# Kernel tuning notes

Measured on AMD Instinct MI355X. Metric: run time of the kernel, lower is better.

The kernel has to match this reference:

```python
import jax, jax.numpy as jnp
import numpy as np

D_MODEL, N_HEAD, D_HEAD = 1024, 16, 64
QLEN, MLEN, BSZ = 1024, 512, 4
KLEN = QLEN + MLEN
RLEN = QLEN + KLEN
SCALE = 1.0 / (D_HEAD ** 0.5)
LN_EPS = 1e-12


def rel_shift(x, klen):
    # x: [i, j, b, n] -> shifted [i, klen, b, n]
    i, j, b, n = x.shape
    x = x.reshape(j, i, b, n)[1:].reshape(i, j - 1, b, n)
    return x[:, :klen]


def layer_norm(x, gamma, beta, eps=LN_EPS):
    mu = jnp.mean(x, axis=-1, keepdims=True)
    var = jnp.mean(jnp.square(x - mu), axis=-1, keepdims=True)
    return (x - mu) * jax.lax.rsqrt(var + eps) * gamma + beta


def setup_inputs() -> dict:
    key = jax.random.key(0)
    ks = jax.random.split(key, 16)
    std = 0.02
    h = jax.random.normal(ks[0], (QLEN, BSZ, D_MODEL), jnp.float32)
    r = jax.random.normal(ks[1], (RLEN, BSZ, D_MODEL), jnp.float32)
    mems = jax.random.normal(ks[2], (MLEN, BSZ, D_MODEL), jnp.float32)
    # binary float mask (1 = masked), broadcast over head dim
    attn_mask = (jax.random.uniform(ks[3], (QLEN, KLEN, BSZ, 1)) < 0.1).astype(jnp.float32)
    # one-hot segment matrix over 2 segment classes
    seg_ids = jax.random.randint(ks[4], (QLEN, KLEN, BSZ), 0, 2)
    seg_mat = jax.nn.one_hot(seg_ids, 2, dtype=jnp.float32)
    Wq = std * jax.random.normal(ks[5], (D_MODEL, N_HEAD, D_HEAD), jnp.float32)
    Wk = std * jax.random.normal(ks[6], (D_MODEL, N_HEAD, D_HEAD), jnp.float32)
    Wv = std * jax.random.normal(ks[7], (D_MODEL, N_HEAD, D_HEAD), jnp.float32)
    Wo = std * jax.random.normal(ks[8], (D_MODEL, N_HEAD, D_HEAD), jnp.float32)
    Wr = std * jax.random.normal(ks[9], (D_MODEL, N_HEAD, D_HEAD), jnp.float32)
    r_w_bias = jnp.zeros((N_HEAD, D_HEAD), jnp.float32)
    r_r_bias = jnp.zeros((N_HEAD, D_HEAD), jnp.float32)
    r_s_bias = jnp.zeros((N_HEAD, D_HEAD), jnp.float32)
    seg_embed = std * jax.random.normal(ks[10], (2, N_HEAD, D_HEAD), jnp.float32)
    ln_gamma = jnp.ones((D_MODEL,), jnp.float32)
    ln_beta = jnp.zeros((D_MODEL,), jnp.float32)
    return dict(h=h, r=r, mems=mems, attn_mask=attn_mask, seg_mat=seg_mat,
                Wq=Wq, Wk=Wk, Wv=Wv, Wo=Wo, Wr=Wr,
                r_w_bias=r_w_bias, r_r_bias=r_r_bias, r_s_bias=r_s_bias,
                seg_embed=seg_embed, ln_gamma=ln_gamma, ln_beta=ln_beta)


def reference(h, r, mems, attn_mask, seg_mat, Wq, Wk, Wv, Wo, Wr,
              r_w_bias, r_r_bias, r_s_bias, seg_embed, ln_gamma, ln_beta):
    cat = jnp.concatenate([mems, h], axis=0)  # [klen, b, d_model]
    q_head = jnp.einsum('ibh,hnd->ibnd', h, Wq)
    k_head_h = jnp.einsum('jbh,hnd->jbnd', cat, Wk)
    v_head_h = jnp.einsum('jbh,hnd->jbnd', cat, Wv)
    k_head_r = jnp.einsum('jbh,hnd->jbnd', r, Wr)

    klen = k_head_h.shape[0]
    ac = jnp.einsum('ibnd,jbnd->ijbn', q_head + r_w_bias, k_head_h)
    bd = jnp.einsum('ibnd,jbnd->ijbn', q_head + r_r_bias, k_head_r)
    bd = rel_shift(bd, klen)
    ef = jnp.einsum('ibnd,snd->ibns', q_head + r_s_bias, seg_embed)
    ef = jnp.einsum('ijbs,ibns->ijbn', seg_mat, ef)

    attn_score = (ac + bd + ef) * SCALE - 1e30 * attn_mask
    attn_prob = jax.nn.softmax(attn_score, axis=1)
    attn_vec = jnp.einsum('ijbn,jbnd->ibnd', attn_prob, v_head_h)

    attn_out = jnp.einsum('ibnd,hnd->ibh', attn_vec, Wo) + h  # residual
    return layer_norm(attn_out, ln_gamma, ln_beta)
```

## Files before the change

### kernel.cpp

```cpp
#include <hip/hip_runtime.h>

typedef unsigned short u16;
typedef __attribute__((ext_vector_type(8))) short bf16x8;
typedef __attribute__((ext_vector_type(4))) float f32x4;

constexpr int DM = 1024;
constexpr int NH = 16;
constexpr int DH = 64;
constexpr int QL = 1024;
constexpr int ML = 512;
constexpr int KL = 1536;
constexpr int RL = 2560;
constexpr int BS = 4;
constexpr int JT = KL / 64;
constexpr float SCALE = 0.125f;

static __device__ __forceinline__ u16 f2bf(float f) {
    unsigned u = __float_as_uint(f);
    u += 0x7fffu + ((u >> 16) & 1u);
    return (u16)(u >> 16);
}

static __device__ __forceinline__ void glds16(const u16* g, u16* l) {
    __builtin_amdgcn_global_load_lds(
        (const __attribute__((address_space(1))) unsigned int*)g,
        (__attribute__((address_space(3))) unsigned int*)l,
        16, 0, 0);
}

__global__ __launch_bounds__(256) void prep_kernel(
    const float* __restrict__ mems, const float* __restrict__ h,
    const float* __restrict__ r, const float* __restrict__ Wo,
    const float* __restrict__ mask, const float* __restrict__ segm,
    const float* __restrict__ Wq, const float* __restrict__ Wk,
    const float* __restrict__ Wv, const float* __restrict__ Wr,
    u16* __restrict__ catb, u16* __restrict__ rb, u16* __restrict__ wob,
    u16* __restrict__ WqT, u16* __restrict__ WkT,
    u16* __restrict__ WvT, u16* __restrict__ WrT,
    ulonglong2* __restrict__ pk)
{
    __shared__ float smem[64 * 65];
    const int id = blockIdx.x;
    const int t = threadIdx.x;

    if (id < 17408) {
        const long C0 = (long)ML * BS * DM;
        const long C1 = (long)KL * BS * DM;
        const long C2 = C1 + (long)RL * BS * DM;
        long g = ((long)id * 256 + t) * 4;
        const float* src; u16* dst;
        if (g < C0)      { src = mems + g;        dst = catb + g; }
        else if (g < C1) { src = h + (g - C0);    dst = catb + g; }
        else if (g < C2) { src = r + (g - C1);    dst = rb + (g - C1); }
        else             { src = Wo + (g - C2);   dst = wob + (g - C2); }
        float4 v = *(const float4*)src;
        unsigned lo = (unsigned)f2bf(v.x) | ((unsigned)f2bf(v.y) << 16);
        unsigned hi = (unsigned)f2bf(v.z) | ((unsigned)f2bf(v.w) << 16);
        *(uint2*)dst = make_uint2(lo, hi);
        return;
    }
    if (id < 18432) {
        float (*tile)[65] = (float(*)[65])smem;
        const int local = id - 17408;
        const float* W; u16* WT;
        switch (local >> 8) {
            case 0:  W = Wq; WT = WqT; break;
            case 1:  W = Wk; WT = WkT; break;
            case 2:  W = Wv; WT = WvT; break;
            default: W = Wr; WT = WrT; break;
        }
        const int k0 = (local & 15) * 64, n0 = ((local >> 4) & 15) * 64;
        const int tr = t >> 6, tc = t & 63;
        #pragma unroll
        for (int rr = 0; rr < 16; rr++) {
            int rw = tr + rr * 4;
            tile[rw][tc] = W[(size_t)(k0 + rw) * DM + n0 + tc];
        }
        __syncthreads();
        #pragma unroll
        for (int rr = 0; rr < 16; rr++) {
            int n = tr + rr * 4;
            WT[(size_t)(n0 + n) * DM + k0 + tc] = f2bf(tile[tc][n]);
        }
        return;
    }
    {
        float* mk = smem;
        float* sg = smem + 256;
        const int local = id - 18432;
        const int i = local / JT, jt = local - i * JT;
        const size_t base = ((size_t)i * KL + jt * 64) * BS;
        mk[t] = mask[base + t];
        float2 s2 = ((const float2*)(segm + base * 2))[t];
        sg[t] = s2.y;
        __syncthreads();
        const int b = t >> 6, lane = t & 63;
        const unsigned long long mb = __ballot(mk[lane * 4 + b] > 0.5f);
        const unsigned long long sb = __ballot(sg[lane * 4 + b] > 0.5f);
        if (lane == 0) {
            ulonglong2 v; v.x = mb; v.y = sb;
            pk[((size_t)b * QL + i) * JT + jt] = v;
        }
    }
}

__global__ __launch_bounds__(256) void proj_kernel(
    const u16* __restrict__ hb, const u16* __restrict__ catb,
    const u16* __restrict__ rb,
    const u16* __restrict__ WqT, const u16* __restrict__ WkT,
    const u16* __restrict__ WvT, const u16* __restrict__ WrT,
    float* __restrict__ q_s, u16* __restrict__ k_s,
    u16* __restrict__ v_s, u16* __restrict__ kr_s)
{
    __shared__ u16 a_lds[128][32];
    __shared__ u16 b_lds[128][32];
    const int id = blockIdx.x;
    const u16 *A, *B; void* C; int SEQ, MODE, local;
    if (id < 256)       { A = hb;   B = WqT; C = q_s;  SEQ = QL; MODE = 1; local = id; }
    else if (id < 640)  { A = catb; B = WkT; C = k_s;  SEQ = KL; MODE = 2; local = id - 256; }
    else if (id < 1024) { A = catb; B = WvT; C = v_s;  SEQ = KL; MODE = 2; local = id - 640; }
    else                { A = rb;   B = WrT; C = kr_s; SEQ = RL; MODE = 2; local = id - 1024; }
    const int bm = local >> 3, bnn = local & 7;

    const int t = threadIdx.x;
    const int w = t >> 6, lane = t & 63, l15 = lane & 15, q4 = lane >> 4;
    const int wm = (w >> 1) * 64, wn = (w & 1) * 64;
    const int srow = w * 32 + (lane >> 2);
    const int scol = (lane & 3) * 8;
    const u16* Ab = A + (size_t)(bm * 128 + srow) * DM + scol;
    const u16* Bb = B + (size_t)(bnn * 128 + srow) * DM + scol;
    u16* a_dst = &a_lds[w * 32][0];
    u16* b_dst = &b_lds[w * 32][0];

    f32x4 acc[4][4] = {};

    for (int k0 = 0; k0 < DM; k0 += 32) {
        __syncthreads();
        glds16(Ab + k0,           a_dst);
        glds16(Ab + k0 + 16 * DM, a_dst + 16 * 32);
        glds16(Bb + k0,           b_dst);
        glds16(Bb + k0 + 16 * DM, b_dst + 16 * 32);
        __syncthreads();
        bf16x8 af[4], bf[4];
        #pragma unroll
        for (int rt = 0; rt < 4; rt++)
            af[rt] = *(const bf16x8*)&a_lds[wm + rt * 16 + l15][q4 * 8];
        #pragma unroll
        for (int ct = 0; ct < 4; ct++)
            bf[ct] = *(const bf16x8*)&b_lds[wn + ct * 16 + l15][q4 * 8];
        #pragma unroll
        for (int rt = 0; rt < 4; rt++)
            #pragma unroll
            for (int ct = 0; ct < 4; ct++)
                acc[rt][ct] = __builtin_amdgcn_mfma_f32_16x16x32_bf16(
                    af[rt], bf[ct], acc[rt][ct], 0, 0, 0);
    }

    #pragma unroll
    for (int rt = 0; rt < 4; rt++)
      #pragma unroll
      for (int ct = 0; ct < 4; ct++)
        #pragma unroll
        for (int rg = 0; rg < 4; rg++) {
            const int R = bm * 128 + wm + rt * 16 + q4 * 4 + rg;
            const int Cc = bnn * 128 + wn + ct * 16 + l15;
            const float v = acc[rt][ct][rg];
            const int sq = R >> 2, bb = R & 3, hn = Cc >> 6, dd = Cc & 63;
            const size_t idx = ((size_t)(bb * NH + hn) * SEQ + sq) * DH + dd;
            if (MODE == 1) ((float*)C)[idx] = v;
            else           ((u16*)C)[idx]  = f2bf(v);
        }
}

__global__ __launch_bounds__(256) void vtrans_kernel(
    const u16* __restrict__ v_s, u16* __restrict__ vt_s)
{
    __shared__ u16 tl[64][72];
    const int j0 = blockIdx.x * 64;
    const int bn = blockIdx.y;
    const u16* vin = v_s + (size_t)bn * KL * DH;
    u16* vout = vt_s + (size_t)bn * DH * KL;
    const int t = threadIdx.x;
    const int r = t >> 3, c8 = (t & 7) * 8;
    #pragma unroll
    for (int it = 0; it < 64; it += 32)
        *(uint4*)&tl[r + it][c8] = *(const uint4*)(vin + (size_t)(j0 + r + it) * DH + c8);
    __syncthreads();
    #pragma unroll
    for (int it = 0; it < 64; it += 32) {
        const int d = r + it;
        u16 tmp[8];
        #pragma unroll
        for (int jj = 0; jj < 8; jj++) tmp[jj] = tl[c8 + jj][d];
        *(uint4*)&vout[(size_t)d * KL + j0 + c8] = *(const uint4*)tmp;
    }
}

__global__ __launch_bounds__(256) void ogemm_kernel(
    const u16* __restrict__ A, const u16* __restrict__ B,
    float* __restrict__ Cout)
{
    __shared__ u16 a_lds[128][32];
    __shared__ u16 b_lds[128][32];
    const int bm = blockIdx.x, bnn = blockIdx.y;
    const int t = threadIdx.x;
    const int w = t >> 6, lane = t & 63, l15 = lane & 15, q4 = lane >> 4;
    const int wm = (w >> 1) * 64, wn = (w & 1) * 64;
    const int srow = w * 32 + (lane >> 2);
    const int scol = (lane & 3) * 8;
    const u16* Ab = A + (size_t)(bm * 128 + srow) * DM + scol;
    const u16* Bb = B + (size_t)(bnn * 128 + srow) * DM + scol;
    u16* a_dst = &a_lds[w * 32][0];
    u16* b_dst = &b_lds[w * 32][0];

    f32x4 acc[4][4] = {};

    for (int k0 = 0; k0 < DM; k0 += 32) {
        __syncthreads();
        glds16(Ab + k0,           a_dst);
        glds16(Ab + k0 + 16 * DM, a_dst + 16 * 32);
        glds16(Bb + k0,           b_dst);
        glds16(Bb + k0 + 16 * DM, b_dst + 16 * 32);
        __syncthreads();
        bf16x8 af[4], bf[4];
        #pragma unroll
        for (int rt = 0; rt < 4; rt++)
            af[rt] = *(const bf16x8*)&a_lds[wm + rt * 16 + l15][q4 * 8];
        #pragma unroll
        for (int ct = 0; ct < 4; ct++)
            bf[ct] = *(const bf16x8*)&b_lds[wn + ct * 16 + l15][q4 * 8];
        #pragma unroll
        for (int rt = 0; rt < 4; rt++)
            #pragma unroll
            for (int ct = 0; ct < 4; ct++)
                acc[rt][ct] = __builtin_amdgcn_mfma_f32_16x16x32_bf16(
                    af[rt], bf[ct], acc[rt][ct], 0, 0, 0);
    }

    #pragma unroll
    for (int rt = 0; rt < 4; rt++)
      #pragma unroll
      for (int ct = 0; ct < 4; ct++)
        #pragma unroll
        for (int rg = 0; rg < 4; rg++) {
            const int R = bm * 128 + wm + rt * 16 + q4 * 4 + rg;
            const int C = bnn * 128 + wn + ct * 16 + l15;
            Cout[(size_t)R * DM + C] = acc[rt][ct][rg];
        }
}

#define FBAR() do { asm volatile("" ::: "memory");  \
                    __builtin_amdgcn_s_barrier();   \
                    asm volatile("" ::: "memory"); } while (0)

#define STAGE(JT_IDX, KB, VB, KRB, MPC)                                        \
  {                                                                            \
    const int j2_ = (JT_IDX) * 64;                                             \
    const int Pb_ = j2_ + QL - i0 - 63;                                        \
    glds16(kg + (size_t)j2_ * DH,      &KB[0][w * 16][0]);                     \
    glds16(kg + (size_t)j2_ * DH + 32, &KB[1][w * 16][0]);                     \
    glds16(vg + j2_,                   &VB[0][w * 16][0]);                     \
    glds16(vg + j2_ + 32,              &VB[1][w * 16][0]);                     \
    const u16* krg_ = kr_bn + (size_t)(Pb_ + w * 32 + krow) * DH + ksrcseg * 8;\
    _Pragma("unroll")                                                          \
    for (int m_ = 0; m_ < 4; m_++)                                             \
      glds16(krg_ + (size_t)m_ * 8 * DH, &KRB[w * 32 + m_ * 8][0]);            \
    _Pragma("unroll")                                                          \
    for (int rg_ = 0; rg_ < 4; rg_++)                                          \
      MPC[rg_] = pk_b[(size_t)(ib + q4 * 4 + rg_) * JT + (JT_IDX)];            \
  }

#define ATTN_STEP(JT_IDX, KB, VB, KRB, MPC)                                    \
  {                                                                            \
    const int jt_ = (JT_IDX);                                                  \
                                      \
    f32x4 sac[4] = {};                                                         \
    _Pragma("unroll")                                                          \
    for (int ct = 0; ct < 4; ct++) {                                           \
      bf16x8 kb0 = *(const bf16x8*)&KB[0][ct * 16 + l15][(q4 ^ ksw) * 8];      \
      bf16x8 kb1 = *(const bf16x8*)&KB[1][ct * 16 + l15][(q4 ^ ksw) * 8];      \
      sac[ct] = __builtin_amdgcn_mfma_f32_16x16x32_bf16(qw[0], kb0, sac[ct], 0, 0, 0); \
      sac[ct] = __builtin_amdgcn_mfma_f32_16x16x32_bf16(qw[1], kb1, sac[ct], 0, 0, 0); \
    }                                                                          \
                    \
    f32x4 bacc[5] = {};                                                        \
    _Pragma("unroll")                                                          \
    for (int wc = 0; wc < 5; wc++) {                                           \
      bf16x8 b0 = *(const bf16x8*)&KRB[lrb + wc * 16][sA];                     \
      bf16x8 b1 = *(const bf16x8*)&KRB[lrb + wc * 16][sB];                     \
      bacc[wc] = __builtin_amdgcn_mfma_f32_16x16x32_bf16(qr[0], b0, bacc[wc], 0, 0, 0); \
      bacc[wc] = __builtin_amdgcn_mfma_f32_16x16x32_bf16(qr[1], b1, bacc[wc], 0, 0, 0); \
    }                                                                          \
                 \
    _Pragma("unroll")                                                          \
    for (int rg = 0; rg < 4; rg++) {                                           \
      const int row = q4 * 4 + rg;                                             \
      const int v = l15 + 15 - row;                             \
      const int srcl = (q4 << 4) | (v & 15);                                   \
      float sh[5];                                                             \
      _Pragma("unroll")                                                        \
      for (int w5 = 0; w5 < 5; w5++)                                           \
        sh[w5] = __shfl(bacc[w5][rg], srcl, 64);                               \
      const float e0 = e_lds[0][w * 16 + row];                                 \
      const float e1 = e_lds[1][w * 16 + row];                                 \
      float s0 = 0.f;                                                          \
      _Pragma("unroll")                                                        \
      for (int ct = 0; ct < 4; ct++) {                                         \
        const float bd = (v < 16) ? sh[ct] : sh[ct + 1];                       \
        const int bit = ct * 16 + l15;                                         \
        const float ef = ((MPC[rg].y >> bit) & 1ull) ? e1 : e0;                \
        const float s = (sac[ct][rg] + bd + ef) * SCALE;                       \
        float p = __expf(s);                                                   \
        p = ((MPC[rg].x >> bit) & 1ull) ? 0.f : p;             \
        const int pg = (2 * ct + (l15 >> 3)) ^ (row & 7);                      \
        p_lds[w][row][pg * 8 + (l15 & 7)] = f2bf(p);                           \
        s0 += p;                                                               \
      }                                                                        \
      l_r[rg] += s0;                                                           \
    }                                                                          \
                   \
    _Pragma("unroll")                                                          \
    for (int kk = 0; kk < 2; kk++) {                                           \
      const int pgr = ((kk * 4 + q4) ^ (l15 & 7)) * 8;                         \
      bf16x8 pf = *(const bf16x8*)&p_lds[w][l15][pgr];                         \
      _Pragma("unroll")                                                        \
      for (int dt = 0; dt < 4; dt++) {                                         \
        bf16x8 vf = *(const bf16x8*)&VB[kk][dt * 16 + l15][(q4 ^ ksw) * 8];    \
        o[dt] = __builtin_amdgcn_mfma_f32_16x16x32_bf16(pf, vf, o[dt], 0, 0, 0); \
      }                                                                        \
    }                                                                          \
                                           \
    if (jt_ < JT - 1) {                                                        \
      FBAR();                                 \
      if (jt_ + 2 < JT) {                                                      \
        STAGE(jt_ + 2, KB, VB, KRB, MPC);       \
        asm volatile("s_waitcnt vmcnt(12)" ::: "memory");     \
      } else {                                                                 \
        asm volatile("s_waitcnt vmcnt(0)" ::: "memory");                       \
      }                                                                        \
      FBAR();                                 \
    }                                                                          \
  }

__global__ __launch_bounds__(256, 2) void attn_kernel(
    const float* __restrict__ q_s, const u16* __restrict__ k_s,
    const u16* __restrict__ vt_s, const u16* __restrict__ kr_s,
    const ulonglong2* __restrict__ pk,
    const float* __restrict__ rwb, const float* __restrict__ rrb,
    const float* __restrict__ rsb, const float* __restrict__ seg_embed,
    u16* __restrict__ av_s)
{
    __shared__ u16 k2[2][2][64][32];
    __shared__ u16 vt2[2][2][64][32];
    __shared__ u16 krl[2][128][64];
    __shared__ u16 p_lds[4][16][64];
    __shared__ float e_lds[2][64];

    const int bn = blockIdx.x;
    const int itile = blockIdx.y;
    const int b = bn >> 4, n = bn & 15;
    const int t = threadIdx.x;
    const int w = t >> 6, lane = t & 63, l15 = lane & 15, q4 = lane >> 4;
    const int i0 = itile * 64;
    const int ib = i0 + w * 16;

    const float* q_bn = q_s + (size_t)bn * QL * DH;
    const u16* k_bn   = k_s  + (size_t)bn * KL * DH;
    const u16* vt_bn  = vt_s + (size_t)bn * DH * KL;
    const u16* kr_bn  = kr_s + (size_t)bn * RL * DH;
    const ulonglong2* pk_b = pk + (size_t)b * QL * JT;

    if (t < 128) {
        const int rr = t >> 1, s = t & 1;
        const float* qrow = q_bn + (size_t)(i0 + rr) * DH;
        const float* se = seg_embed + (s * NH + n) * DH;
        const float* bias = rsb + n * DH;
        float acc = 0.f;
        #pragma unroll 16
        for (int d = 0; d < DH; d++) acc += (qrow[d] + bias[d]) * se[d];
        e_lds[s][rr] = acc;
    }

    bf16x8 qw[2], qr[2];
    {
        const float* qrow = q_bn + (size_t)(ib + l15) * DH;
        const float* bw = rwb + n * DH;
        const float* br = rrb + n * DH;
        #pragma unroll
        for (int kk = 0; kk < 2; kk++) {
            const int dbase = kk * 32 + q4 * 8;
            #pragma unroll
            for (int j = 0; j < 8; j++) {
                float qv = qrow[dbase + j];
                qw[kk][j] = (short)f2bf(qv + bw[dbase + j]);
                qr[kk][j] = (short)f2bf(qv + br[dbase + j]);
            }
        }
    }

    const int srow = lane >> 2;
    const int ssw  = ((lane & 3) ^ ((srow >> 1) & 3)) * 8;
    const u16* kg = k_bn  + (size_t)(w * 16 + srow) * DH + ssw;
    const u16* vg = vt_bn + (size_t)(w * 16 + srow) * KL + ssw;

    const int krow = lane >> 3;
    const int ksrcseg = (lane & 7) ^ krow;

    const int lrb = 48 - w * 16 + l15;
    const int sA = ((q4)     ^ (l15 & 7)) * 8;
    const int sB = ((q4 + 4) ^ (l15 & 7)) * 8;
    const int ksw = (l15 >> 1) & 3;

    f32x4 o[4] = {};
    float l_r[4] = {0.f, 0.f, 0.f, 0.f};
    ulonglong2 mpA[4], mpB[4];

    STAGE(0, k2[0], vt2[0], krl[0], mpA);
    STAGE(1, k2[1], vt2[1], krl[1], mpB);
    asm volatile("s_waitcnt vmcnt(12) lgkmcnt(0)" ::: "memory");
    FBAR();

    #pragma unroll 1
    for (int jt0 = 0; jt0 < JT; jt0 += 2) {
        ATTN_STEP(jt0,     k2[0], vt2[0], krl[0], mpA);
        ATTN_STEP(jt0 + 1, k2[1], vt2[1], krl[1], mpB);
    }

    #pragma unroll
    for (int rg = 0; rg < 4; rg++) {
        #pragma unroll
        for (int off = 1; off < 16; off <<= 1)
            l_r[rg] += __shfl_xor(l_r[rg], off, 64);
        l_r[rg] = 1.f / l_r[rg];
    }
    #pragma unroll
    for (int dt = 0; dt < 4; dt++)
        #pragma unroll
        for (int rg = 0; rg < 4; rg++) {
            const int row = q4 * 4 + rg;
            const int ii = ib + row;
            const int d = dt * 16 + l15;
            const float v = o[dt][rg] * l_r[rg];
            av_s[(size_t)(ii * BS + b) * DM + n * DH + d] = f2bf(v);
        }
}

__global__ __launch_bounds__(256) void ln_kernel(
    const float* __restrict__ ao, const float* __restrict__ h,
    const float* __restrict__ gamma, const float* __restrict__ beta,
    float* __restrict__ out)
{
    __shared__ float red[8];
    const int row = blockIdx.x, t = threadIdx.x;
    const float* a  = ao + (size_t)row * DM;
    const float* hh = h  + (size_t)row * DM;
    float4 av = *(const float4*)(a + t * 4);
    float4 hv = *(const float4*)(hh + t * 4);
    const float x0 = av.x + hv.x, x1 = av.y + hv.y;
    const float x2 = av.z + hv.z, x3 = av.w + hv.w;
    float s = x0 + x1 + x2 + x3;
    float s2 = x0 * x0 + x1 * x1 + x2 * x2 + x3 * x3;
    #pragma unroll
    for (int off = 1; off < 64; off <<= 1) {
        s  += __shfl_xor(s, off, 64);
        s2 += __shfl_xor(s2, off, 64);
    }
    const int w = t >> 6;
    if ((t & 63) == 0) { red[w] = s; red[4 + w] = s2; }
    __syncthreads();
    s  = red[0] + red[1] + red[2] + red[3];
    s2 = red[4] + red[5] + red[6] + red[7];
    const float mu = s * (1.f / DM);
    const float var = s2 * (1.f / DM) - mu * mu;
    const float rstd = rsqrtf(var + 1e-12f);
    float4 g  = *(const float4*)(gamma + t * 4);
    float4 bb = *(const float4*)(beta + t * 4);
    float4 ov;
    ov.x = (x0 - mu) * rstd * g.x + bb.x;
    ov.y = (x1 - mu) * rstd * g.y + bb.y;
    ov.z = (x2 - mu) * rstd * g.z + bb.z;
    ov.w = (x3 - mu) * rstd * g.w + bb.w;
    *(float4*)(out + (size_t)row * DM + t * 4) = ov;
}

extern "C" void kernel_launch(void* const* d_in, const int* in_sizes, int n_in,
                              void* d_out, int out_size, void* d_ws, size_t ws_size,
                              hipStream_t stream) {
    (void)in_sizes; (void)n_in; (void)out_size; (void)ws_size;
    const float* h    = (const float*)d_in[0];
    const float* r    = (const float*)d_in[1];
    const float* mems = (const float*)d_in[2];
    const float* mask = (const float*)d_in[3];
    const float* segm = (const float*)d_in[4];
    const float* Wq   = (const float*)d_in[5];
    const float* Wk   = (const float*)d_in[6];
    const float* Wv   = (const float*)d_in[7];
    const float* Wo   = (const float*)d_in[8];
    const float* Wr   = (const float*)d_in[9];
    const float* rwb  = (const float*)d_in[10];
    const float* rrb  = (const float*)d_in[11];
    const float* rsb  = (const float*)d_in[12];
    const float* semb = (const float*)d_in[13];
    const float* gam  = (const float*)d_in[14];
    const float* bet  = (const float*)d_in[15];
    float* out = (float*)d_out;

    char* wsb = (char*)d_ws;
    size_t off = 0;
    auto alloc = [&](size_t bytes) -> void* {
        void* p = wsb + off; off += (bytes + 255) & ~(size_t)255; return p;
    };
    u16* catb = (u16*)alloc((size_t)KL * BS * DM * 2);
    u16* rb   = (u16*)alloc((size_t)RL * BS * DM * 2);
    u16* WqT  = (u16*)alloc((size_t)DM * DM * 2);
    u16* WkT  = (u16*)alloc((size_t)DM * DM * 2);
    u16* WvT  = (u16*)alloc((size_t)DM * DM * 2);
    u16* WrT  = (u16*)alloc((size_t)DM * DM * 2);
    u16* WoB  = (u16*)alloc((size_t)DM * DM * 2);
    float* q_s = (float*)alloc((size_t)BS * NH * QL * DH * 4);
    u16* k_s  = (u16*)alloc((size_t)BS * NH * KL * DH * 2);
    u16* vt_s = (u16*)alloc((size_t)BS * NH * KL * DH * 2);
    u16* kr_s = (u16*)alloc((size_t)BS * NH * RL * DH * 2 + 8192);
    u16* av_s = (u16*)alloc((size_t)QL * BS * DM * 2);
    float* ao_s = (float*)alloc((size_t)QL * BS * DM * 4);
    ulonglong2* pk = (ulonglong2*)alloc((size_t)BS * QL * JT * 16);
    u16* v_s = (u16*)ao_s;

    prep_kernel<<<43008, 256, 0, stream>>>(mems, h, r, Wo, mask, segm,
                                           Wq, Wk, Wv, Wr,
                                           catb, rb, WoB,
                                           WqT, WkT, WvT, WrT, pk);
    const u16* hb = catb + (size_t)2048 * DM;
    proj_kernel<<<1664, 256, 0, stream>>>(hb, catb, rb, WqT, WkT, WvT, WrT,
                                          q_s, k_s, v_s, kr_s);
    vtrans_kernel<<<dim3(JT, 64), 256, 0, stream>>>(v_s, vt_s);
    attn_kernel<<<dim3(64, 16), 256, 0, stream>>>(q_s, k_s, vt_s, kr_s, pk,
                                                  rwb, rrb, rsb, semb, av_s);
    ogemm_kernel<<<dim3(32, 8), 256, 0, stream>>>(av_s, WoB, ao_s);
    ln_kernel<<<4096, 256, 0, stream>>>(ao_s, h, gam, bet, out);
}
```

Before: 499.9 us.

## Restructure attention staging: rolling KR panels, direct V loads, LDS mask bits

```diff
diff --git a/kernel.cpp b/kernel.cpp
--- a/kernel.cpp
+++ b/kernel.cpp
@@ -14,6 +14,7 @@
 constexpr int BS = 4;
 constexpr int JT = KL / 64;
 constexpr float SCALE = 0.125f;
+constexpr float SC2 = 0.125f * 1.4426950408889634f;
 
 static __device__ __forceinline__ u16 f2bf(float f) {
     unsigned u = __float_as_uint(f);
@@ -253,27 +254,38 @@
                     __builtin_amdgcn_s_barrier();   \
                     asm volatile("" ::: "memory"); } while (0)
 
-#define STAGE(JT_IDX, KB, VB, KRB, MPC)                                        \
+#define STAGE_KR(PANEL_IDX, DST)                                               \
   {                                                                            \
-    const int j2_ = (JT_IDX) * 64;                                             \
-    const int Pb_ = j2_ + QL - i0 - 63;                                        \
-    glds16(kg + (size_t)j2_ * DH,      &KB[0][w * 16][0]);                     \
-    glds16(kg + (size_t)j2_ * DH + 32, &KB[1][w * 16][0]);                     \
-    glds16(vg + j2_,                   &VB[0][w * 16][0]);                     \
-    glds16(vg + j2_ + 32,              &VB[1][w * 16][0]);                     \
-    const u16* krg_ = kr_bn + (size_t)(Pb_ + w * 32 + krow) * DH + ksrcseg * 8;\
-    _Pragma("unroll")                                                          \
-    for (int m_ = 0; m_ < 4; m_++)                                             \
-      glds16(krg_ + (size_t)m_ * 8 * DH, &KRB[w * 32 + m_ * 8][0]);            \
-    _Pragma("unroll")                                                          \
-    for (int rg_ = 0; rg_ < 4; rg_++)                                          \
-      MPC[rg_] = pk_b[(size_t)(ib + q4 * 4 + rg_) * JT + (JT_IDX)];            \
+    const int br_ = QL - i0 - 63 + (PANEL_IDX) * 64 + w * 16 + krow;           \
+    glds16(kr_bn + (size_t)br_ * DH + ksrcseg * 8,       (DST) + (w*16)*64);   \
+    glds16(kr_bn + (size_t)(br_ + 8) * DH + ksrcseg * 8, (DST) + (w*16+8)*64); \
   }
 
-#define ATTN_STEP(JT_IDX, KB, VB, KRB, MPC)                                    \
+#define STAGE_K(TI, KB, PKB)                                                   \
+  {                                                                            \
+    glds16(kg + (size_t)(TI) * 64 * DH,      &KB[0][w * 16][0]);               \
+    glds16(kg + (size_t)(TI) * 64 * DH + 32, &KB[1][w * 16][0]);               \
+    glds16((const u16*)&pk_b[(size_t)(i0 + lane) * JT + (TI)], (u16*)&PKB[0]); \
+  }
+
+#define ATTN_STEP(JT_IDX, KB, PKB)                                             \
   {                                                                            \
     const int jt_ = (JT_IDX);                                                  \
+    const int j0_ = jt_ * 64;                                                  \
+       \
+    bf16x8 vf[2][4];                                                           \
+    {                                                                          \
+      const u16* vb_ = vt_bn + (size_t)l15 * KL + j0_ + q4 * 8;                \
+      _Pragma("unroll")                                                        \
+      for (int dt = 0; dt < 4; dt++) {                                         \
+        vf[0][dt] = *(const bf16x8*)(vb_ + (size_t)(dt * 16) * KL);            \
+        vf[1][dt] = *(const bf16x8*)(vb_ + (size_t)(dt * 16) * KL + 32);       \
+      }                                                                        \
+    }                                                                          \
+                 \
+    if (jt_ < JT - 1) STAGE_KR(jt_ + 2, krC_);                                 \
                                       \
+    __builtin_amdgcn_s_setprio(1);                                             \
     f32x4 sac[4] = {};                                                         \
     _Pragma("unroll")                                                          \
     for (int ct = 0; ct < 4; ct++) {                                           \
@@ -282,19 +294,25 @@
       sac[ct] = __builtin_amdgcn_mfma_f32_16x16x32_bf16(qw[0], kb0, sac[ct], 0, 0, 0); \
       sac[ct] = __builtin_amdgcn_mfma_f32_16x16x32_bf16(qw[1], kb1, sac[ct], 0, 0, 0); \
     }                                                                          \
-                    \
+                     \
     f32x4 bacc[5] = {};                                                        \
     _Pragma("unroll")                                                          \
     for (int wc = 0; wc < 5; wc++) {                                           \
-      bf16x8 b0 = *(const bf16x8*)&KRB[lrb + wc * 16][sA];                     \
-      bf16x8 b1 = *(const bf16x8*)&KRB[lrb + wc * 16][sB];                     \
+      const int c_ = 48 - w * 16 + wc * 16;                                    \
+      const u16* pr_ = ((c_ >> 6) ? krB_ : krA_) + ((c_ & 63) + l15) * 64;     \
+      bf16x8 b0 = *(const bf16x8*)(pr_ + sA);                                  \
+      bf16x8 b1 = *(const bf16x8*)(pr_ + sB);                                  \
       bacc[wc] = __builtin_amdgcn_mfma_f32_16x16x32_bf16(qr[0], b0, bacc[wc], 0, 0, 0); \
       bacc[wc] = __builtin_amdgcn_mfma_f32_16x16x32_bf16(qr[1], b1, bacc[wc], 0, 0, 0); \
     }                                                                          \
+    __builtin_amdgcn_s_setprio(0);                                             \
                  \
     _Pragma("unroll")                                                          \
     for (int rg = 0; rg < 4; rg++) {                                           \
       const int row = q4 * 4 + rg;                                             \
+      const ulonglong2 mp = PKB[w * 16 + row];                                 \
+      const unsigned long long mx = mp.x >> l15;                               \
+      const unsigned long long sy = mp.y >> l15;                               \
       const int v = l15 + 15 - row;                             \
       const int srcl = (q4 << 4) | (v & 15);                                   \
       float sh[5];                                                             \
@@ -307,42 +325,41 @@
       _Pragma("unroll")                                                        \
       for (int ct = 0; ct < 4; ct++) {                                         \
         const float bd = (v < 16) ? sh[ct] : sh[ct + 1];                       \
-        const int bit = ct * 16 + l15;                                         \
-        const float ef = ((MPC[rg].y >> bit) & 1ull) ? e1 : e0;                \
-        const float s = (sac[ct][rg] + bd + ef) * SCALE;                       \
-        float p = __expf(s);                                                   \
-        p = ((MPC[rg].x >> bit) & 1ull) ? 0.f : p;             \
+        const float ef = ((sy >> (ct * 16)) & 1ull) ? e1 : e0;                 \
+        float p = exp2f((sac[ct][rg] + bd + ef) * SC2);                        \
+        p = ((mx >> (ct * 16)) & 1ull) ? 0.f : p;              \
         const int pg = (2 * ct + (l15 >> 3)) ^ (row & 7);                      \
         p_lds[w][row][pg * 8 + (l15 & 7)] = f2bf(p);                           \
         s0 += p;                                                               \
       }                                                                        \
       l_r[rg] += s0;                                                           \
     }                                                                          \
-                   \
+            \
+    __builtin_amdgcn_s_setprio(1);                                             \
     _Pragma("unroll")                                                          \
     for (int kk = 0; kk < 2; kk++) {                                           \
       const int pgr = ((kk * 4 + q4) ^ (l15 & 7)) * 8;                         \
       bf16x8 pf = *(const bf16x8*)&p_lds[w][l15][pgr];                         \
       _Pragma("unroll")                                                        \
-      for (int dt = 0; dt < 4; dt++) {                                         \
-        bf16x8 vf = *(const bf16x8*)&VB[kk][dt * 16 + l15][(q4 ^ ksw) * 8];    \
-        o[dt] = __builtin_amdgcn_mfma_f32_16x16x32_bf16(pf, vf, o[dt], 0, 0, 0); \
-      }                                                                        \
+      for (int dt = 0; dt < 4; dt++)                                           \
+        o[dt] = __builtin_amdgcn_mfma_f32_16x16x32_bf16(pf, vf[kk][dt], o[dt], 0, 0, 0); \
     }                                                                          \
+    __builtin_amdgcn_s_setprio(0);                                             \
                                            \
     if (jt_ < JT - 1) {                                                        \
       FBAR();                                 \
       if (jt_ + 2 < JT) {                                                      \
-        STAGE(jt_ + 2, KB, VB, KRB, MPC);       \
-        asm volatile("s_waitcnt vmcnt(12)" ::: "memory");     \
+        STAGE_K(jt_ + 2, KB, PKB);               \
+        asm volatile("s_waitcnt vmcnt(3)" ::: "memory");                       \
       } else {                                                                 \
         asm volatile("s_waitcnt vmcnt(0)" ::: "memory");                       \
       }                                                                        \
       FBAR();                                 \
     }                                                                          \
+    { u16* t_ = krA_; krA_ = krB_; krB_ = krC_; krC_ = t_; }                   \
   }
 
-__global__ __launch_bounds__(256, 2) void attn_kernel(
+__global__ __launch_bounds__(256, 3) void attn_kernel(
     const float* __restrict__ q_s, const u16* __restrict__ k_s,
     const u16* __restrict__ vt_s, const u16* __restrict__ kr_s,
     const ulonglong2* __restrict__ pk,
@@ -351,9 +368,9 @@
     u16* __restrict__ av_s)
 {
     __shared__ u16 k2[2][2][64][32];
-    __shared__ u16 vt2[2][2][64][32];
-    __shared__ u16 krl[2][128][64];
+    __shared__ u16 krp[3][64][64];
     __shared__ u16 p_lds[4][16][64];
+    __shared__ ulonglong2 pk_lds[2][64];
     __shared__ float e_lds[2][64];
 
     const int bn = blockIdx.x;
@@ -400,30 +417,33 @@
 
     const int srow = lane >> 2;
     const int ssw  = ((lane & 3) ^ ((srow >> 1) & 3)) * 8;
-    const u16* kg = k_bn  + (size_t)(w * 16 + srow) * DH + ssw;
-    const u16* vg = vt_bn + (size_t)(w * 16 + srow) * KL + ssw;
+    const u16* kg = k_bn + (size_t)(w * 16 + srow) * DH + ssw;
 
     const int krow = lane >> 3;
     const int ksrcseg = (lane & 7) ^ krow;
 
-    const int lrb = 48 - w * 16 + l15;
     const int sA = ((q4)     ^ (l15 & 7)) * 8;
     const int sB = ((q4 + 4) ^ (l15 & 7)) * 8;
     const int ksw = (l15 >> 1) & 3;
 
+    u16* krA_ = &krp[0][0][0];
+    u16* krB_ = &krp[1][0][0];
+    u16* krC_ = &krp[2][0][0];
+
     f32x4 o[4] = {};
     float l_r[4] = {0.f, 0.f, 0.f, 0.f};
-    ulonglong2 mpA[4], mpB[4];
-
-    STAGE(0, k2[0], vt2[0], krl[0], mpA);
-    STAGE(1, k2[1], vt2[1], krl[1], mpB);
-    asm volatile("s_waitcnt vmcnt(12) lgkmcnt(0)" ::: "memory");
+
+    STAGE_KR(0, krA_);
+    STAGE_KR(1, krB_);
+    STAGE_K(0, k2[0], pk_lds[0]);
+    STAGE_K(1, k2[1], pk_lds[1]);
+    asm volatile("s_waitcnt vmcnt(3) lgkmcnt(0)" ::: "memory");
     FBAR();
 
     #pragma unroll 1
     for (int jt0 = 0; jt0 < JT; jt0 += 2) {
-        ATTN_STEP(jt0,     k2[0], vt2[0], krl[0], mpA);
-        ATTN_STEP(jt0 + 1, k2[1], vt2[1], krl[1], mpB);
+        ATTN_STEP(jt0,     k2[0], pk_lds[0]);
+        ATTN_STEP(jt0 + 1, k2[1], pk_lds[1]);
     }
 
     #pragma unroll
```

Result: slower. 805.4 us (+61.1%).
